# Performance work log

Measured on AMD Instinct MI355X. Metric: run time of the kernel, lower is better.

Reference implementation:

```python
import jax, jax.numpy as jnp
import numpy as np

N = 8192      # total QM atoms (concatenated over batch)
L = 6         # num_interactions / trajectory length
F = 256       # hidden_size
FH = F // 2
D_RBF = 32    # distance_embedding_size
E = 131072    # total probe edges
P = 32768     # total probes
CUTOFF = 4.0


def silu(x):
    return x * jax.nn.sigmoid(x)


def setup_inputs() -> dict:
    key = jax.random.key(0)
    ks = jax.random.split(key, 20)
    g = lambda k, shp, s=1.0: jax.random.normal(k, shp, dtype=jnp.float32) * s
    s_stack = g(ks[0], (N, L, F))
    v_stack = g(ks[1], (N, L, 3, F))
    # positions in a 2A box so all probe-atom distances < cutoff=4A
    atom_xyz = jax.random.uniform(ks[2], (N, 3), dtype=jnp.float32) * 2.0
    probe_xyz = jax.random.uniform(ks[3], (P, 3), dtype=jnp.float32) * 2.0
    cell = jnp.eye(3, dtype=jnp.float32) * 2.0
    probe_edges_displacement = jnp.zeros((E, 3), dtype=jnp.float32)
    atom_idx = jax.random.randint(ks[4], (E,), 0, N)
    probe_idx = jax.random.randint(ks[5], (E,), 0, P)
    probe_edges = jnp.stack([atom_idx, probe_idx], axis=1)
    in_dim = D_RBF + 3 * F  # e_pi || q_pi || n_i || S_JK
    return {
        's_stack': s_stack,
        'v_stack': v_stack,
        'atom_xyz': atom_xyz,
        'probe_xyz': probe_xyz,
        'cell': cell,
        'probe_edges_displacement': probe_edges_displacement,
        # JK attention MLP: F -> F/2 -> 1
        'attn_w1': g(ks[6], (F, FH), 1.0 / np.sqrt(F)),
        'attn_b1': jnp.zeros((FH,), jnp.float32),
        'attn_w2': g(ks[7], (FH, 1), 1.0 / np.sqrt(FH)),
        'attn_b2': jnp.zeros((1,), jnp.float32),
        # readout msg MLP: (D_rbf+3F) -> F -> F/2 -> 1
        'msg_w1': g(ks[8], (in_dim, F), 1.0 / np.sqrt(in_dim)),
        'msg_b1': jnp.zeros((F,), jnp.float32),
        'msg_w2': g(ks[9], (F, FH), 1.0 / np.sqrt(F)),
        'msg_b2': jnp.zeros((FH,), jnp.float32),
        'msg_w3': g(ks[10], (FH, 1), 1.0 / np.sqrt(FH)),
        'msg_b3': jnp.zeros((1,), jnp.float32),
        'probe_edges': probe_edges,
    }


def reference(s_stack, v_stack, atom_xyz, probe_xyz, cell, probe_edges_displacement,
              attn_w1, attn_b1, attn_w2, attn_b2,
              msg_w1, msg_b1, msg_w2, msg_b2, msg_w3, msg_b3,
              probe_edges):
    # ---- JKNetAggregation: node-level attention over layer trajectory ----
    h = silu(jnp.einsum('nlf,fh->nlh', s_stack, attn_w1) + attn_b1)   # [N,L,F/2]
    logits = (jnp.einsum('nlh,ho->nlo', h, attn_w2) + attn_b2)[..., 0]  # [N,L]
    a = jax.nn.softmax(logits, axis=1)                                  # [N,L]
    S_JK = jnp.einsum('nl,nlf->nf', a, s_stack)                         # [N,F]
    V_JK = jnp.einsum('nl,nlcf->ncf', a, v_stack)                       # [N,3,F]

    # ---- InfoBottleneckReadout: gather -> per-edge MLP -> scatter ----
    atom_idx = probe_edges[:, 0]
    probe_idx = probe_edges[:, 1]
    shift = probe_edges_displacement @ cell                             # [E,3] PBC shift
    diff = probe_xyz[probe_idx] - (atom_xyz[atom_idx] + shift)          # [E,3]
    dist = jnp.linalg.norm(diff, axis=-1)                               # [E]
    d = dist[:, None]
    n = jnp.arange(1, D_RBF + 1, dtype=jnp.float32)
    e_pi = jnp.sin(d * n * jnp.pi / CUTOFF) / (d + 1e-8)                # [E,D_rbf] sinc RBF
    r_hat = diff / (d + 1e-8)                                           # [E,3]
    V_e = V_JK[atom_idx]                                                # [E,3,F]
    q_pi = jnp.einsum('ecf,ec->ef', V_e, r_hat)                         # [E,F]
    n_i = jnp.linalg.norm(V_JK, axis=1)                                 # [N,F]
    h_pi = jnp.concatenate([e_pi, q_pi, n_i[atom_idx], S_JK[atom_idx]], axis=-1)  # [E,D_rbf+3F]
    m = silu(h_pi @ msg_w1 + msg_b1)
    m = silu(m @ msg_w2 + msg_b2)
    m = (m @ msg_w3 + msg_b3)[:, 0]                                     # [E]
    cw = jnp.where(dist < CUTOFF, 0.5 * (jnp.cos(jnp.pi * dist / CUTOFF) + 1.0), 0.0)
    rho = jax.ops.segment_sum(m * cw, probe_idx, num_segments=P)        # [P]
    return rho
```

## Files before the change

### kernel.cpp

```cpp
#include <hip/hip_runtime.h>
#include <math.h>
#include <stdint.h>


#define L_DIM 6
#define F_DIM 256
#define FH_DIM 128
#define DRBF 32
#define CUTOFF_F 4.0f
#define PI_F 3.14159265358979323846f

using bf16x8 = __attribute__((ext_vector_type(8))) short;
using f32x4v = __attribute__((ext_vector_type(4))) float;

__device__ __forceinline__ float silu_f(float x){ return x / (1.f + __expf(-x)); }

__device__ __forceinline__ unsigned short f2bf(float f){
    uint32_t u = __float_as_uint(f);
    uint32_t r = (u + 0x7fffu + ((u >> 16) & 1u)) >> 16;
    return (unsigned short)r;
}

__global__ __launch_bounds__(256) void kPrep(
    const float* __restrict__ msg_w1, const float* __restrict__ msg_w2,
    const float* __restrict__ attn_w1,
    unsigned short* __restrict__ w1bt, unsigned short* __restrict__ w1cdt,
    unsigned short* __restrict__ w2t, unsigned short* __restrict__ wA1t)
{
    int idx = blockIdx.x * 256 + threadIdx.x;
    if (idx < 65536){
        int k = idx >> 8, j = idx & 255;
        w1bt[(size_t)j * 256 + k] = f2bf(msg_w1[(size_t)(DRBF + k) * F_DIM + j]);
    } else if (idx < 196608){
        int i2 = idx - 65536;
        int k = i2 >> 8, j = i2 & 255;
        w1cdt[(size_t)j * 512 + k] = f2bf(msg_w1[(size_t)(DRBF + 256 + k) * F_DIM + j]);
    } else if (idx < 229376){
        int i3 = idx - 196608;
        int k = i3 >> 7, h = i3 & 127;
        w2t[(size_t)h * 256 + k] = f2bf(msg_w2[(size_t)k * FH_DIM + h]);
    } else {
        int i4 = idx - 229376;
        int j = i4 >> 8, k = i4 & 255;
        wA1t[(size_t)j * 256 + k] = f2bf(attn_w1[(size_t)k * FH_DIM + j]);
    }
}

__global__ __launch_bounds__(256) void kL(
    const float* __restrict__ s2d, const unsigned short* __restrict__ wA1t,
    const float* __restrict__ attn_b1, const float* __restrict__ attn_w2,
    float* __restrict__ LG)
{
    __shared__ float part[4][64];

    const int t  = threadIdx.x;
    const int l  = t & 63;
    const int w  = t >> 6;
    const int lm = l & 15, lq = l >> 4;

    bf16x8 bfr[2][8];
    #pragma unroll
    for (int nt2 = 0; nt2 < 2; nt2++){
        const int col = w*32 + nt2*16 + lm;
        #pragma unroll
        for (int kb = 0; kb < 8; kb++)
            bfr[nt2][kb] = *(const bf16x8*)(wA1t + (size_t)col * 256 + kb*32 + lq*8);
    }
    const float b1a = attn_b1[w*32 + lm];
    const float b1b = attn_b1[w*32 + 16 + lm];
    const float w2a = attn_w2[w*32 + lm];
    const float w2b = attn_w2[w*32 + 16 + lm];

    const int r00 = blockIdx.x * 64;

    #pragma unroll
    for (int mt = 0; mt < 4; mt++){
        const int r0 = r00 + mt * 16;
        bf16x8 af[8];
        #pragma unroll
        for (int kb = 0; kb < 8; kb++){
            const float* ap = s2d + (size_t)(r0 + lm) * 256 + kb*32 + lq*8;
            float4 fa = *(const float4*)ap;
            float4 fb = *(const float4*)(ap + 4);
            bf16x8 v;
            v[0] = (short)f2bf(fa.x); v[1] = (short)f2bf(fa.y);
            v[2] = (short)f2bf(fa.z); v[3] = (short)f2bf(fa.w);
            v[4] = (short)f2bf(fb.x); v[5] = (short)f2bf(fb.y);
            v[6] = (short)f2bf(fb.z); v[7] = (short)f2bf(fb.w);
            af[kb] = v;
        }
        f32x4v a0 = {0.f,0.f,0.f,0.f}, a1 = {0.f,0.f,0.f,0.f};
        #pragma unroll
        for (int kb = 0; kb < 8; kb++){
            a0 = __builtin_amdgcn_mfma_f32_16x16x32_bf16(af[kb], bfr[0][kb], a0, 0, 0, 0);
            a1 = __builtin_amdgcn_mfma_f32_16x16x32_bf16(af[kb], bfr[1][kb], a1, 0, 0, 0);
        }
        #pragma unroll
        for (int r = 0; r < 4; r++){
            float p = silu_f(a0[r] + b1a) * w2a + silu_f(a1[r] + b1b) * w2b;
            #pragma unroll
            for (int m = 8; m >= 1; m >>= 1) p += __shfl_xor(p, m, 64);
            if (lm == 0) part[w][mt*16 + lq*4 + r] = p;
        }
    }
    __syncthreads();
    if (t < 64)
        LG[r00 + t] = part[0][t] + part[1][t] + part[2][t] + part[3][t];
}

__global__ __launch_bounds__(256) void kW(
    const float* __restrict__ s_stack, const float* __restrict__ v_stack,
    const float* __restrict__ LG,
    unsigned short* __restrict__ VJKb, unsigned short* __restrict__ NISb, int N)
{
    const int t    = threadIdx.x;
    const int w    = t >> 6;
    const int lane = t & 63;
    const int n    = min(blockIdx.x * 4 + w, N - 1);

    float aw[L_DIM];
    #pragma unroll
    for (int l = 0; l < L_DIM; l++) aw[l] = LG[(size_t)n * L_DIM + l];
    float mx = aw[0];
    #pragma unroll
    for (int l = 1; l < L_DIM; l++) mx = fmaxf(mx, aw[l]);
    float sum = 0.f;
    #pragma unroll
    for (int l = 0; l < L_DIM; l++){ aw[l] = __expf(aw[l] - mx); sum += aw[l]; }
    const float inv = 1.f / sum;
    #pragma unroll
    for (int l = 0; l < L_DIM; l++) aw[l] *= inv;

    const float* sp = s_stack + (size_t)n * (L_DIM * F_DIM) + lane * 4;
    const float* vp = v_stack + (size_t)n * (L_DIM * 3 * F_DIM) + lane * 4;
    float4 v0 = {0.f,0.f,0.f,0.f}, v1 = {0.f,0.f,0.f,0.f}, v2 = {0.f,0.f,0.f,0.f};
    float4 sj = {0.f,0.f,0.f,0.f};
    #pragma unroll
    for (int l = 0; l < L_DIM; l++){
        const float a = aw[l];
        float4 ss = *(const float4*)(sp + (size_t)l * F_DIM);
        float4 x0 = *(const float4*)(vp + (size_t)(l*3+0) * F_DIM);
        float4 x1 = *(const float4*)(vp + (size_t)(l*3+1) * F_DIM);
        float4 x2 = *(const float4*)(vp + (size_t)(l*3+2) * F_DIM);
        v0.x = fmaf(a, x0.x, v0.x); v0.y = fmaf(a, x0.y, v0.y);
        v0.z = fmaf(a, x0.z, v0.z); v0.w = fmaf(a, x0.w, v0.w);
        v1.x = fmaf(a, x1.x, v1.x); v1.y = fmaf(a, x1.y, v1.y);
        v1.z = fmaf(a, x1.z, v1.z); v1.w = fmaf(a, x1.w, v1.w);
        v2.x = fmaf(a, x2.x, v2.x); v2.y = fmaf(a, x2.y, v2.y);
        v2.z = fmaf(a, x2.z, v2.z); v2.w = fmaf(a, x2.w, v2.w);
        sj.x = fmaf(a, ss.x, sj.x); sj.y = fmaf(a, ss.y, sj.y);
        sj.z = fmaf(a, ss.z, sj.z); sj.w = fmaf(a, ss.w, sj.w);
    }
    float4 ni;
    ni.x = sqrtf(v0.x*v0.x + v1.x*v1.x + v2.x*v2.x);
    ni.y = sqrtf(v0.y*v0.y + v1.y*v1.y + v2.y*v2.y);
    ni.z = sqrtf(v0.z*v0.z + v1.z*v1.z + v2.z*v2.z);
    ni.w = sqrtf(v0.w*v0.w + v1.w*v1.w + v2.w*v2.w);

    ushort4 o;
    o = (ushort4){f2bf(v0.x), f2bf(v0.y), f2bf(v0.z), f2bf(v0.w)};
    *(ushort4*)&VJKb[((size_t)n*3 + 0) * F_DIM + lane*4] = o;
    o = (ushort4){f2bf(v1.x), f2bf(v1.y), f2bf(v1.z), f2bf(v1.w)};
    *(ushort4*)&VJKb[((size_t)n*3 + 1) * F_DIM + lane*4] = o;
    o = (ushort4){f2bf(v2.x), f2bf(v2.y), f2bf(v2.z), f2bf(v2.w)};
    *(ushort4*)&VJKb[((size_t)n*3 + 2) * F_DIM + lane*4] = o;
    o = (ushort4){f2bf(ni.x), f2bf(ni.y), f2bf(ni.z), f2bf(ni.w)};
    *(ushort4*)&NISb[(size_t)n * 512 + lane*4] = o;
    o = (ushort4){f2bf(sj.x), f2bf(sj.y), f2bf(sj.z), f2bf(sj.w)};
    *(ushort4*)&NISb[(size_t)n * 512 + 256 + lane*4] = o;
}

__global__ __launch_bounds__(256) void kA2u(
    const unsigned short* __restrict__ VJKb, const unsigned short* __restrict__ w1bt,
    float* __restrict__ UT4, int M)
{
    const int t  = threadIdx.x;
    const int l  = t & 63;
    const int w  = t >> 6;
    const int lm = l & 15, lq = l >> 4;

    bf16x8 bfr[4][8];
    #pragma unroll
    for (int ct = 0; ct < 4; ct++)
        #pragma unroll
        for (int kb = 0; kb < 8; kb++)
            bfr[ct][kb] = *(const bf16x8*)(w1bt + (size_t)(w*64 + ct*16 + lm) * 256 + kb*32 + lq*8);

    const int r00 = blockIdx.x * 128;
    #pragma unroll 1
    for (int mt = 0; mt < 8; mt++){
        const int r0 = r00 + mt * 16;
        bf16x8 af[8];
        #pragma unroll
        for (int kb = 0; kb < 8; kb++)
            af[kb] = *(const bf16x8*)(VJKb + (size_t)(r0 + lm) * 256 + kb*32 + lq*8);
        f32x4v acc[4];
        #pragma unroll
        for (int ct = 0; ct < 4; ct++) acc[ct] = (f32x4v){0.f,0.f,0.f,0.f};
        #pragma unroll
        for (int kb = 0; kb < 8; kb++)
            #pragma unroll
            for (int ct = 0; ct < 4; ct++)
                acc[ct] = __builtin_amdgcn_mfma_f32_16x16x32_bf16(af[kb], bfr[ct][kb], acc[ct], 0, 0, 0);
        #pragma unroll
        for (int ct = 0; ct < 4; ct++){
            const int col = w*64 + ct*16 + lm;
            #pragma unroll
            for (int r = 0; r < 4; r++){
                const int row = r0 + lq*4 + r;
                const int n = row / 3, c = row - n*3;
                UT4[(((size_t)n << 8) + col) * 4 + c] = acc[ct][r];
            }
        }
    }
}

__global__ __launch_bounds__(256) void kA2t(
    const unsigned short* __restrict__ NISb, const unsigned short* __restrict__ w1cdt,
    const float* __restrict__ msg_b1,
    float* __restrict__ UT4, int M)
{
    const int t  = threadIdx.x;
    const int l  = t & 63;
    const int w  = t >> 6;
    const int lm = l & 15, lq = l >> 4;

    const int ch = blockIdx.x & 1;
    const int bm = blockIdx.x >> 1;

    bf16x8 bfr[2][16];
    #pragma unroll
    for (int ct = 0; ct < 2; ct++)
        #pragma unroll
        for (int kb = 0; kb < 16; kb++)
            bfr[ct][kb] = *(const bf16x8*)(w1cdt + (size_t)(ch*128 + w*32 + ct*16 + lm) * 512 + kb*32 + lq*8);

    const int r00 = bm * 128;
    #pragma unroll 1
    for (int mt = 0; mt < 8; mt++){
        const int r0 = r00 + mt * 16;
        bf16x8 af[16];
        #pragma unroll
        for (int kb = 0; kb < 16; kb++)
            af[kb] = *(const bf16x8*)(NISb + (size_t)(r0 + lm) * 512 + kb*32 + lq*8);
        f32x4v acc[2];
        #pragma unroll
        for (int ct = 0; ct < 2; ct++) acc[ct] = (f32x4v){0.f,0.f,0.f,0.f};
        #pragma unroll
        for (int kb = 0; kb < 16; kb++)
            #pragma unroll
            for (int ct = 0; ct < 2; ct++)
                acc[ct] = __builtin_amdgcn_mfma_f32_16x16x32_bf16(af[kb], bfr[ct][kb], acc[ct], 0, 0, 0);
        #pragma unroll
        for (int ct = 0; ct < 2; ct++){
            const int col = ch*128 + w*32 + ct*16 + lm;
            const float bias = msg_b1[col];
            #pragma unroll
            for (int r = 0; r < 4; r++){
                const int n = r0 + lq*4 + r;
                UT4[(((size_t)n << 8) + col) * 4 + 3] = acc[ct][r] + bias;
            }
        }
    }
}

__global__ __launch_bounds__(256) void kHist(const int* __restrict__ pe, int* __restrict__ cnt, int E){
    int e = blockIdx.x * 256 + threadIdx.x;
    if (e < E) atomicAdd(&cnt[pe[(size_t)e*2]], 1);
}

__global__ __launch_bounds__(1024) void kScan(const int* __restrict__ cnt, int* __restrict__ off, int N){
    __shared__ int sums[1024];
    const int t = threadIdx.x;
    const int base = t * 8;
    int c[8]; int s = 0;
    #pragma unroll
    for (int j = 0; j < 8; j++){
        int v = (base + j < N) ? cnt[base + j] : 0;
        c[j] = s; s += v;
    }
    sums[t] = s;
    __syncthreads();
    for (int d = 1; d < 1024; d <<= 1){
        int v = (t >= d) ? sums[t - d] : 0;
        __syncthreads();
        sums[t] += v;
        __syncthreads();
    }
    int excl = (t == 0) ? 0 : sums[t - 1];
    #pragma unroll
    for (int j = 0; j < 8; j++)
        if (base + j < N) off[base + j] = excl + c[j];
    if (t == 1023) off[N] = sums[1023];
}

__global__ __launch_bounds__(256) void kScatter(const int* __restrict__ pe,
    const int* __restrict__ off, int* __restrict__ pos, int* __restrict__ perm, int E){
    int e = blockIdx.x * 256 + threadIdx.x;
    if (e < E){
        int i = pe[(size_t)e*2];
        int slot = atomicAdd(&pos[i], 1);
        perm[off[i] + slot] = e;
    }
}

__global__ __launch_bounds__(256) void kB1(
    const int* __restrict__ pe, const float* __restrict__ disp,
    const float* __restrict__ cell,
    const float* __restrict__ atom_xyz, const float* __restrict__ probe_xyz,
    const float* __restrict__ UT4,
    const float* __restrict__ msg_w1,
    const unsigned short* __restrict__ w2t, const float* __restrict__ msg_b2,
    const float* __restrict__ msg_w3, const float* __restrict__ msg_b3,
    const int* __restrict__ perm,
    float* __restrict__ rho, int E)
{
    __shared__ unsigned short x_lds[32 * 256];
    __shared__ unsigned short epi_b[32 * 40];
    __shared__ int   ai_l[32];
    __shared__ int   pp_l[32];
    __shared__ float4 rc4_l[32];
    __shared__ float part[4][32];

    char* xbase = (char*)x_lds;

    const int t  = threadIdx.x;
    const int l  = t & 63;
    const int w  = t >> 6;
    const int lq = l >> 4;
    const int lm = l & 15;

    const float c0 = cell[0], c1 = cell[1], c2 = cell[2];
    const float c3 = cell[3], c4 = cell[4], c5 = cell[5];
    const float c6 = cell[6], c7 = cell[7], c8 = cell[8];

    bf16x8 w1afr[4];
    #pragma unroll
    for (int nt = 0; nt < 4; nt++){
        const int col = w*64 + nt*16 + lm;
        bf16x8 v;
        #pragma unroll
        for (int j = 0; j < 8; j++)
            v[j] = (short)f2bf(msg_w1[(size_t)(lq*8 + j) * F_DIM + col]);
        w1afr[nt] = v;
    }

    bf16x8 bfr[2][8];
    #pragma unroll
    for (int nt2 = 0; nt2 < 2; nt2++){
        const int h = w*32 + nt2*16 + lm;
        #pragma unroll
        for (int kb = 0; kb < 8; kb++)
            bfr[nt2][kb] = *(const bf16x8*)(w2t + (size_t)h * F_DIM + kb*32 + lq*8);
    }
    const float b2v0 = msg_b2[w*32 + lm];
    const float b2v1 = msg_b2[w*32 + 16 + lm];
    const float w3v0 = msg_w3[w*32 + lm];
    const float w3v1 = msg_w3[w*32 + 16 + lm];
    const float b3   = msg_b3[0];

    const int e0 = blockIdx.x * 128;

    int ee_r[4], ia_r[4], ip_r[4];
    #pragma unroll
    for (int bb = 0; bb < 4; bb++){
        int s = min(e0 + bb*32 + (t >> 3), E - 1);
        ee_r[bb] = perm[s];
    }
    #pragma unroll
    for (int bb = 0; bb < 4; bb++){
        ia_r[bb] = pe[(size_t)ee_r[bb]*2];
        ip_r[bb] = pe[(size_t)ee_r[bb]*2 + 1];
    }

    #pragma unroll 1
    for (int bb = 0; bb < 4; bb++){
        const int e0b = e0 + bb * 32;

        {
            const int slot = t >> 3, q = t & 7;
            const int ee = ee_r[bb];
            const int ia = ia_r[bb];
            const int ip = ip_r[bb];
            const float d0 = disp[(size_t)ee*3], d1 = disp[(size_t)ee*3+1], d2 = disp[(size_t)ee*3+2];
            const float sx = d0*c0 + d1*c3 + d2*c6;
            const float sy = d0*c1 + d1*c4 + d2*c7;
            const float sz = d0*c2 + d1*c5 + d2*c8;
            const float dx = probe_xyz[(size_t)ip*3+0] - (atom_xyz[(size_t)ia*3+0] + sx);
            const float dy = probe_xyz[(size_t)ip*3+1] - (atom_xyz[(size_t)ia*3+1] + sy);
            const float dz = probe_xyz[(size_t)ip*3+2] - (atom_xyz[(size_t)ia*3+2] + sz);
            const float dist = sqrtf(dx*dx + dy*dy + dz*dz);
            const float inv  = 1.f / (dist + 1e-8f);
            const float base = dist * (PI_F / CUTOFF_F);
            ushort4 eb;
            eb.x = f2bf(__sinf(base * (float)(q*4 + 1)) * inv);
            eb.y = f2bf(__sinf(base * (float)(q*4 + 2)) * inv);
            eb.z = f2bf(__sinf(base * (float)(q*4 + 3)) * inv);
            eb.w = f2bf(__sinf(base * (float)(q*4 + 4)) * inv);
            *(ushort4*)&epi_b[slot*40 + q*4] = eb;
            if (q == 0){
                ai_l[slot] = ia;
                pp_l[slot] = ip;
                float cw = (dist < CUTOFF_F) ? 0.5f * (__cosf(base) + 1.f) : 0.f;
                rc4_l[slot] = (float4){dx*inv, dy*inv, dz*inv, cw};
            }
        }
        __syncthreads();

        f32x4v pacc[2][4];
        #pragma unroll
        for (int mt = 0; mt < 2; mt++)
            #pragma unroll
            for (int nt = 0; nt < 4; nt++) pacc[mt][nt] = (f32x4v){0.f,0.f,0.f,0.f};
        #pragma unroll
        for (int mt = 0; mt < 2; mt++){
            const bf16x8 af = *(const bf16x8*)&epi_b[(mt*16 + lm)*40 + lq*8];
            #pragma unroll
            for (int nt = 0; nt < 4; nt++)
                pacc[mt][nt] = __builtin_amdgcn_mfma_f32_16x16x32_bf16(af, w1afr[nt], pacc[mt][nt], 0, 0, 0);
        }

        #pragma unroll
        for (int mt = 0; mt < 2; mt++){
            #pragma unroll
            for (int r = 0; r < 4; r++){
                const int e = mt*16 + lq*4 + r;
                const int i = ai_l[e];
                const float4 rc = rc4_l[e];
                const float* up = UT4 + ((size_t)i << 10);
                #pragma unroll
                for (int nt = 0; nt < 4; nt++){
                    const int col = w*64 + nt*16 + lm;
                    const float4 ut = *(const float4*)(up + (size_t)col * 4);
                    float z = pacc[mt][nt][r] + ut.w;
                    z = fmaf(rc.x, ut.x, fmaf(rc.y, ut.y, fmaf(rc.z, ut.z, z)));
                    const int wofs = e*512 + ((col*2) ^ ((e & 7) << 4));
                    *(unsigned short*)(xbase + wofs) = f2bf(silu_f(z));
                }
            }
        }
        __syncthreads();

        f32x4v acc00 = {0.f,0.f,0.f,0.f}, acc01 = {0.f,0.f,0.f,0.f};
        f32x4v acc10 = {0.f,0.f,0.f,0.f}, acc11 = {0.f,0.f,0.f,0.f};
        const int eA0 = lm;
        const int eA1 = 16 + lm;
        #pragma unroll
        for (int kb = 0; kb < 8; kb++){
            const int ko = kb*64 + lq*16;
            bf16x8 af0 = *(const bf16x8*)(xbase + eA0*512 + (ko ^ ((eA0 & 7) << 4)));
            bf16x8 af1 = *(const bf16x8*)(xbase + eA1*512 + (ko ^ ((eA1 & 7) << 4)));
            acc00 = __builtin_amdgcn_mfma_f32_16x16x32_bf16(af0, bfr[0][kb], acc00, 0, 0, 0);
            acc01 = __builtin_amdgcn_mfma_f32_16x16x32_bf16(af0, bfr[1][kb], acc01, 0, 0, 0);
            acc10 = __builtin_amdgcn_mfma_f32_16x16x32_bf16(af1, bfr[0][kb], acc10, 0, 0, 0);
            acc11 = __builtin_amdgcn_mfma_f32_16x16x32_bf16(af1, bfr[1][kb], acc11, 0, 0, 0);
        }

        float pr0[4], pr1[4];
        #pragma unroll
        for (int r = 0; r < 4; r++){
            pr0[r] = silu_f(acc00[r] + b2v0) * w3v0 + silu_f(acc01[r] + b2v1) * w3v1;
            pr1[r] = silu_f(acc10[r] + b2v0) * w3v0 + silu_f(acc11[r] + b2v1) * w3v1;
        }
        #pragma unroll
        for (int r = 0; r < 4; r++){
            #pragma unroll
            for (int m = 8; m >= 1; m >>= 1){
                pr0[r] += __shfl_xor(pr0[r], m, 64);
                pr1[r] += __shfl_xor(pr1[r], m, 64);
            }
        }
        if (lm == 0){
            #pragma unroll
            for (int r = 0; r < 4; r++){
                part[w][lq*4 + r]      = pr0[r];
                part[w][16 + lq*4 + r] = pr1[r];
            }
        }
        __syncthreads();

        if (t < 32 && (e0b + t) < E){
            float tot = part[0][t] + part[1][t] + part[2][t] + part[3][t] + b3;
            atomicAdd(&rho[pp_l[t]], tot * rc4_l[t].w);
        }
        __syncthreads();
    }
}

extern "C" void kernel_launch(void* const* d_in, const int* in_sizes, int n_in,
                              void* d_out, int out_size, void* d_ws, size_t ws_size,
                              hipStream_t stream)
{
    const float* s_stack   = (const float*)d_in[0];
    const float* v_stack   = (const float*)d_in[1];
    const float* atom_xyz  = (const float*)d_in[2];
    const float* probe_xyz = (const float*)d_in[3];
    const float* cell      = (const float*)d_in[4];
    const float* disp      = (const float*)d_in[5];
    const float* attn_w1   = (const float*)d_in[6];
    const float* attn_b1   = (const float*)d_in[7];
    const float* attn_w2   = (const float*)d_in[8];
    const float* msg_w1    = (const float*)d_in[10];
    const float* msg_b1    = (const float*)d_in[11];
    const float* msg_w2    = (const float*)d_in[12];
    const float* msg_b2    = (const float*)d_in[13];
    const float* msg_w3    = (const float*)d_in[14];
    const float* msg_b3    = (const float*)d_in[15];
    const int*   pe        = (const int*)d_in[16];

    const int N = in_sizes[0] / (L_DIM * F_DIM);
    const int E = in_sizes[16] / 2;
    const int P = out_size;
    const size_t NF = (size_t)N * F_DIM;

    float* ws = (float*)d_ws;
    unsigned short* VJKb = (unsigned short*)ws;
    unsigned short* NISb = VJKb + 3*NF;
    float* UT4 = ws + (5*NF)/2;
    unsigned short* w1bt  = (unsigned short*)(ws + (13*NF)/2);
    unsigned short* w1cdt = w1bt + 65536;
    unsigned short* w2t   = w1cdt + 131072;
    unsigned short* wA1t  = w2t + 32768;
    float* LG  = (float*)(wA1t + 32768);
    int* cnt  = (int*)(LG + (size_t)N * L_DIM);
    int* pos  = cnt + N;
    int* offs = pos + N;
    int* perm = offs + N + 1;

    hipMemsetAsync(d_out, 0, (size_t)P * sizeof(float), stream);
    hipMemsetAsync(cnt, 0, 2 * (size_t)N * sizeof(int), stream);

    kPrep<<<1024, 256, 0, stream>>>(msg_w1, msg_w2, attn_w1, w1bt, w1cdt, w2t, wA1t);

    kL<<<(N * L_DIM) / 64, 256, 0, stream>>>(s_stack, wA1t, attn_b1, attn_w2, LG);
    kW<<<(N + 3) / 4, 256, 0, stream>>>(s_stack, v_stack, LG, VJKb, NISb, N);

    kA2u<<<(3 * N) / 128, 256, 0, stream>>>(VJKb, w1bt, UT4, 3 * N);
    kA2t<<<(N / 128) * 2, 256, 0, stream>>>(NISb, w1cdt, msg_b1, UT4, N);

    const int gE = (E + 255) / 256;
    kHist<<<gE, 256, 0, stream>>>(pe, cnt, E);
    kScan<<<1, 1024, 0, stream>>>(cnt, offs, N);
    kScatter<<<gE, 256, 0, stream>>>(pe, offs, pos, perm, E);

    kB1<<<(E + 127) / 128, 256, 0, stream>>>(pe, disp, cell, atom_xyz, probe_xyz,
                                             UT4, msg_w1,
                                             w2t, msg_b2, msg_w3, msg_b3,
                                             perm, (float*)d_out, E);
}
```

Baseline: 208.1 us.

## Fuse attention logits with JK weighting, merge A2 GEMMs, fold memsets into prep

Merges the layer-attention logit kernel and the weighted JK aggregation kernel into one kernel. The logits for 16 atoms stay in shared memory, which removes the LG buffer round trip and one launch. The two first-layer projection GEMM kernels now run as one launch that branches on block index. The output and count memsets move into the weight prep kernel. This cuts launch overhead and global traffic, but the fused kernel has fewer blocks, so there is less parallelism in the aggregation phase.

Result: faster. 190.4 us (-8.5%).

```diff
diff --git a/kernel.cpp b/kernel.cpp
--- a/kernel.cpp
+++ b/kernel.cpp
@@ -25,7 +25,8 @@
     const float* __restrict__ msg_w1, const float* __restrict__ msg_w2,
     const float* __restrict__ attn_w1,
     unsigned short* __restrict__ w1bt, unsigned short* __restrict__ w1cdt,
-    unsigned short* __restrict__ w2t, unsigned short* __restrict__ wA1t)
+    unsigned short* __restrict__ w2t, unsigned short* __restrict__ wA1t,
+    float* __restrict__ rho, int P, int* __restrict__ cntpos, int CN)
 {
     int idx = blockIdx.x * 256 + threadIdx.x;
     if (idx < 65536){
@@ -39,19 +40,27 @@
         int i3 = idx - 196608;
         int k = i3 >> 7, h = i3 & 127;
         w2t[(size_t)h * 256 + k] = f2bf(msg_w2[(size_t)k * FH_DIM + h]);
-    } else {
+    } else if (idx < 262144){
         int i4 = idx - 229376;
         int j = i4 >> 8, k = i4 & 255;
         wA1t[(size_t)j * 256 + k] = f2bf(attn_w1[(size_t)k * FH_DIM + j]);
-    }
-}
-
-__global__ __launch_bounds__(256) void kL(
-    const float* __restrict__ s2d, const unsigned short* __restrict__ wA1t,
+    } else if (idx < 262144 + 32768){
+        int i5 = idx - 262144;
+        if (i5 < P) rho[i5] = 0.f;
+    } else {
+        int i6 = idx - 262144 - 32768;
+        if (i6 < CN) cntpos[i6] = 0;
+    }
+}
+
+__global__ __launch_bounds__(256) void kAW(
+    const float* __restrict__ s_stack, const float* __restrict__ v_stack,
+    const unsigned short* __restrict__ wA1t,
     const float* __restrict__ attn_b1, const float* __restrict__ attn_w2,
-    float* __restrict__ LG)
+    unsigned short* __restrict__ VJKb, unsigned short* __restrict__ NISb, int N)
 {
-    __shared__ float part[4][64];
+    __shared__ float part[4][96];
+    __shared__ float aw_l[16][8];
 
     const int t  = threadIdx.x;
     const int l  = t & 63;
@@ -71,15 +80,18 @@
     const float w2a = attn_w2[w*32 + lm];
     const float w2b = attn_w2[w*32 + 16 + lm];
 
-    const int r00 = blockIdx.x * 64;
-
-    #pragma unroll
-    for (int mt = 0; mt < 4; mt++){
-        const int r0 = r00 + mt * 16;
+    const int n0 = blockIdx.x * 16;
+    const size_t rbase = (size_t)n0 * L_DIM;
+    const size_t rmax  = (size_t)N * L_DIM - 1;
+
+    #pragma unroll
+    for (int mt = 0; mt < 6; mt++){
+        const size_t r0 = rbase + mt * 16;
         bf16x8 af[8];
         #pragma unroll
         for (int kb = 0; kb < 8; kb++){
-            const float* ap = s2d + (size_t)(r0 + lm) * 256 + kb*32 + lq*8;
+            size_t row = r0 + lm; if (row > rmax) row = rmax;
+            const float* ap = s_stack + row * 256 + kb*32 + lq*8;
             float4 fa = *(const float4*)ap;
             float4 fb = *(const float4*)(ap + 4);
             bf16x8 v;
@@ -104,161 +116,151 @@
         }
     }
     __syncthreads();
-    if (t < 64)
-        LG[r00 + t] = part[0][t] + part[1][t] + part[2][t] + part[3][t];
-}
-
-__global__ __launch_bounds__(256) void kW(
-    const float* __restrict__ s_stack, const float* __restrict__ v_stack,
-    const float* __restrict__ LG,
-    unsigned short* __restrict__ VJKb, unsigned short* __restrict__ NISb, int N)
-{
-    const int t    = threadIdx.x;
-    const int w    = t >> 6;
-    const int lane = t & 63;
-    const int n    = min(blockIdx.x * 4 + w, N - 1);
-
-    float aw[L_DIM];
-    #pragma unroll
-    for (int l = 0; l < L_DIM; l++) aw[l] = LG[(size_t)n * L_DIM + l];
-    float mx = aw[0];
-    #pragma unroll
-    for (int l = 1; l < L_DIM; l++) mx = fmaxf(mx, aw[l]);
-    float sum = 0.f;
-    #pragma unroll
-    for (int l = 0; l < L_DIM; l++){ aw[l] = __expf(aw[l] - mx); sum += aw[l]; }
-    const float inv = 1.f / sum;
-    #pragma unroll
-    for (int l = 0; l < L_DIM; l++) aw[l] *= inv;
-
-    const float* sp = s_stack + (size_t)n * (L_DIM * F_DIM) + lane * 4;
-    const float* vp = v_stack + (size_t)n * (L_DIM * 3 * F_DIM) + lane * 4;
-    float4 v0 = {0.f,0.f,0.f,0.f}, v1 = {0.f,0.f,0.f,0.f}, v2 = {0.f,0.f,0.f,0.f};
-    float4 sj = {0.f,0.f,0.f,0.f};
-    #pragma unroll
-    for (int l = 0; l < L_DIM; l++){
-        const float a = aw[l];
-        float4 ss = *(const float4*)(sp + (size_t)l * F_DIM);
-        float4 x0 = *(const float4*)(vp + (size_t)(l*3+0) * F_DIM);
-        float4 x1 = *(const float4*)(vp + (size_t)(l*3+1) * F_DIM);
-        float4 x2 = *(const float4*)(vp + (size_t)(l*3+2) * F_DIM);
-        v0.x = fmaf(a, x0.x, v0.x); v0.y = fmaf(a, x0.y, v0.y);
-        v0.z = fmaf(a, x0.z, v0.z); v0.w = fmaf(a, x0.w, v0.w);
-        v1.x = fmaf(a, x1.x, v1.x); v1.y = fmaf(a, x1.y, v1.y);
-        v1.z = fmaf(a, x1.z, v1.z); v1.w = fmaf(a, x1.w, v1.w);
-        v2.x = fmaf(a, x2.x, v2.x); v2.y = fmaf(a, x2.y, v2.y);
-        v2.z = fmaf(a, x2.z, v2.z); v2.w = fmaf(a, x2.w, v2.w);
-        sj.x = fmaf(a, ss.x, sj.x); sj.y = fmaf(a, ss.y, sj.y);
-        sj.z = fmaf(a, ss.z, sj.z); sj.w = fmaf(a, ss.w, sj.w);
-    }
-    float4 ni;
-    ni.x = sqrtf(v0.x*v0.x + v1.x*v1.x + v2.x*v2.x);
-    ni.y = sqrtf(v0.y*v0.y + v1.y*v1.y + v2.y*v2.y);
-    ni.z = sqrtf(v0.z*v0.z + v1.z*v1.z + v2.z*v2.z);
-    ni.w = sqrtf(v0.w*v0.w + v1.w*v1.w + v2.w*v2.w);
-
-    ushort4 o;
-    o = (ushort4){f2bf(v0.x), f2bf(v0.y), f2bf(v0.z), f2bf(v0.w)};
-    *(ushort4*)&VJKb[((size_t)n*3 + 0) * F_DIM + lane*4] = o;
-    o = (ushort4){f2bf(v1.x), f2bf(v1.y), f2bf(v1.z), f2bf(v1.w)};
-    *(ushort4*)&VJKb[((size_t)n*3 + 1) * F_DIM + lane*4] = o;
-    o = (ushort4){f2bf(v2.x), f2bf(v2.y), f2bf(v2.z), f2bf(v2.w)};
-    *(ushort4*)&VJKb[((size_t)n*3 + 2) * F_DIM + lane*4] = o;
-    o = (ushort4){f2bf(ni.x), f2bf(ni.y), f2bf(ni.z), f2bf(ni.w)};
-    *(ushort4*)&NISb[(size_t)n * 512 + lane*4] = o;
-    o = (ushort4){f2bf(sj.x), f2bf(sj.y), f2bf(sj.z), f2bf(sj.w)};
-    *(ushort4*)&NISb[(size_t)n * 512 + 256 + lane*4] = o;
-}
-
-__global__ __launch_bounds__(256) void kA2u(
+    if (t < 96) part[0][t] = part[0][t] + part[1][t] + part[2][t] + part[3][t];
+    __syncthreads();
+    if (t < 16){
+        float e[L_DIM]; float mx = -1e30f;
+        #pragma unroll
+        for (int l6 = 0; l6 < L_DIM; l6++) mx = fmaxf(mx, part[0][t*L_DIM + l6]);
+        float s = 0.f;
+        #pragma unroll
+        for (int l6 = 0; l6 < L_DIM; l6++){ e[l6] = __expf(part[0][t*L_DIM + l6] - mx); s += e[l6]; }
+        float inv = 1.f / s;
+        #pragma unroll
+        for (int l6 = 0; l6 < L_DIM; l6++) aw_l[t][l6] = e[l6] * inv;
+    }
+    __syncthreads();
+
+    #pragma unroll 1
+    for (int aa = 0; aa < 4; aa++){
+        const int n = min(n0 + w*4 + aa, N - 1);
+        float aw[L_DIM];
+        #pragma unroll
+        for (int l6 = 0; l6 < L_DIM; l6++) aw[l6] = aw_l[w*4 + aa][l6];
+
+        const float* sp = s_stack + (size_t)n * (L_DIM * F_DIM) + l * 4;
+        const float* vp = v_stack + (size_t)n * (L_DIM * 3 * F_DIM) + l * 4;
+        float4 v0 = {0.f,0.f,0.f,0.f}, v1 = {0.f,0.f,0.f,0.f}, v2 = {0.f,0.f,0.f,0.f};
+        float4 sj = {0.f,0.f,0.f,0.f};
+        #pragma unroll
+        for (int l6 = 0; l6 < L_DIM; l6++){
+            const float a = aw[l6];
+            float4 ss = *(const float4*)(sp + (size_t)l6 * F_DIM);
+            float4 x0 = *(const float4*)(vp + (size_t)(l6*3+0) * F_DIM);
+            float4 x1 = *(const float4*)(vp + (size_t)(l6*3+1) * F_DIM);
+            float4 x2 = *(const float4*)(vp + (size_t)(l6*3+2) * F_DIM);
+            v0.x = fmaf(a, x0.x, v0.x); v0.y = fmaf(a, x0.y, v0.y);
+            v0.z = fmaf(a, x0.z, v0.z); v0.w = fmaf(a, x0.w, v0.w);
+            v1.x = fmaf(a, x1.x, v1.x); v1.y = fmaf(a, x1.y, v1.y);
+            v1.z = fmaf(a, x1.z, v1.z); v1.w = fmaf(a, x1.w, v1.w);
+            v2.x = fmaf(a, x2.x, v2.x); v2.y = fmaf(a, x2.y, v2.y);
+            v2.z = fmaf(a, x2.z, v2.z); v2.w = fmaf(a, x2.w, v2.w);
+            sj.x = fmaf(a, ss.x, sj.x); sj.y = fmaf(a, ss.y, sj.y);
+            sj.z = fmaf(a, ss.z, sj.z); sj.w = fmaf(a, ss.w, sj.w);
+        }
+        float4 ni;
+        ni.x = sqrtf(v0.x*v0.x + v1.x*v1.x + v2.x*v2.x);
+        ni.y = sqrtf(v0.y*v0.y + v1.y*v1.y + v2.y*v2.y);
+        ni.z = sqrtf(v0.z*v0.z + v1.z*v1.z + v2.z*v2.z);
+        ni.w = sqrtf(v0.w*v0.w + v1.w*v1.w + v2.w*v2.w);
+
+        ushort4 o;
+        o = (ushort4){f2bf(v0.x), f2bf(v0.y), f2bf(v0.z), f2bf(v0.w)};
+        *(ushort4*)&VJKb[((size_t)n*3 + 0) * F_DIM + l*4] = o;
+        o = (ushort4){f2bf(v1.x), f2bf(v1.y), f2bf(v1.z), f2bf(v1.w)};
+        *(ushort4*)&VJKb[((size_t)n*3 + 1) * F_DIM + l*4] = o;
+        o = (ushort4){f2bf(v2.x), f2bf(v2.y), f2bf(v2.z), f2bf(v2.w)};
+        *(ushort4*)&VJKb[((size_t)n*3 + 2) * F_DIM + l*4] = o;
+        o = (ushort4){f2bf(ni.x), f2bf(ni.y), f2bf(ni.z), f2bf(ni.w)};
+        *(ushort4*)&NISb[(size_t)n * 512 + l*4] = o;
+        o = (ushort4){f2bf(sj.x), f2bf(sj.y), f2bf(sj.z), f2bf(sj.w)};
+        *(ushort4*)&NISb[(size_t)n * 512 + 256 + l*4] = o;
+    }
+}
+
+__global__ __launch_bounds__(256) void kA2(
     const unsigned short* __restrict__ VJKb, const unsigned short* __restrict__ w1bt,
-    float* __restrict__ UT4, int M)
+    const unsigned short* __restrict__ NISb, const unsigned short* __restrict__ w1cdt,
+    const float* __restrict__ msg_b1,
+    float* __restrict__ UT4, int gU)
 {
     const int t  = threadIdx.x;
     const int l  = t & 63;
     const int w  = t >> 6;
     const int lm = l & 15, lq = l >> 4;
 
-    bf16x8 bfr[4][8];
-    #pragma unroll
-    for (int ct = 0; ct < 4; ct++)
-        #pragma unroll
-        for (int kb = 0; kb < 8; kb++)
-            bfr[ct][kb] = *(const bf16x8*)(w1bt + (size_t)(w*64 + ct*16 + lm) * 256 + kb*32 + lq*8);
-
-    const int r00 = blockIdx.x * 128;
-    #pragma unroll 1
-    for (int mt = 0; mt < 8; mt++){
-        const int r0 = r00 + mt * 16;
-        bf16x8 af[8];
-        #pragma unroll
-        for (int kb = 0; kb < 8; kb++)
-            af[kb] = *(const bf16x8*)(VJKb + (size_t)(r0 + lm) * 256 + kb*32 + lq*8);
-        f32x4v acc[4];
-        #pragma unroll
-        for (int ct = 0; ct < 4; ct++) acc[ct] = (f32x4v){0.f,0.f,0.f,0.f};
-        #pragma unroll
-        for (int kb = 0; kb < 8; kb++)
-            #pragma unroll
-            for (int ct = 0; ct < 4; ct++)
-                acc[ct] = __builtin_amdgcn_mfma_f32_16x16x32_bf16(af[kb], bfr[ct][kb], acc[ct], 0, 0, 0);
-        #pragma unroll
-        for (int ct = 0; ct < 4; ct++){
-            const int col = w*64 + ct*16 + lm;
-            #pragma unroll
-            for (int r = 0; r < 4; r++){
-                const int row = r0 + lq*4 + r;
-                const int n = row / 3, c = row - n*3;
-                UT4[(((size_t)n << 8) + col) * 4 + c] = acc[ct][r];
+    if ((int)blockIdx.x < gU){
+        bf16x8 bfr[4][8];
+        #pragma unroll
+        for (int ct = 0; ct < 4; ct++)
+            #pragma unroll
+            for (int kb = 0; kb < 8; kb++)
+                bfr[ct][kb] = *(const bf16x8*)(w1bt + (size_t)(w*64 + ct*16 + lm) * 256 + kb*32 + lq*8);
+
+        const int r00 = blockIdx.x * 128;
+        #pragma unroll 1
+        for (int mt = 0; mt < 8; mt++){
+            const int r0 = r00 + mt * 16;
+            bf16x8 af[8];
+            #pragma unroll
+            for (int kb = 0; kb < 8; kb++)
+                af[kb] = *(const bf16x8*)(VJKb + (size_t)(r0 + lm) * 256 + kb*32 + lq*8);
+            f32x4v acc[4];
+            #pragma unroll
+            for (int ct = 0; ct < 4; ct++) acc[ct] = (f32x4v){0.f,0.f,0.f,0.f};
+            #pragma unroll
+            for (int kb = 0; kb < 8; kb++)
+                #pragma unroll
+                for (int ct = 0; ct < 4; ct++)
+                    acc[ct] = __builtin_amdgcn_mfma_f32_16x16x32_bf16(af[kb], bfr[ct][kb], acc[ct], 0, 0, 0);
+            #pragma unroll
+            for (int ct = 0; ct < 4; ct++){
+                const int col = w*64 + ct*16 + lm;
+                #pragma unroll
+                for (int r = 0; r < 4; r++){
+                    const int row = r0 + lq*4 + r;
+                    const int n = row / 3, c = row - n*3;
+                    UT4[(((size_t)n << 8) + col) * 4 + c] = acc[ct][r];
+                }
             }
         }
-    }
-}
-
-__global__ __launch_bounds__(256) void kA2t(
-    const unsigned short* __restrict__ NISb, const unsigned short* __restrict__ w1cdt,
-    const float* __restrict__ msg_b1,
-    float* __restrict__ UT4, int M)
-{
-    const int t  = threadIdx.x;
-    const int l  = t & 63;
-    const int w  = t >> 6;
-    const int lm = l & 15, lq = l >> 4;
-
-    const int ch = blockIdx.x & 1;
-    const int bm = blockIdx.x >> 1;
-
-    bf16x8 bfr[2][16];
-    #pragma unroll
-    for (int ct = 0; ct < 2; ct++)
-        #pragma unroll
-        for (int kb = 0; kb < 16; kb++)
-            bfr[ct][kb] = *(const bf16x8*)(w1cdt + (size_t)(ch*128 + w*32 + ct*16 + lm) * 512 + kb*32 + lq*8);
-
-    const int r00 = bm * 128;
-    #pragma unroll 1
-    for (int mt = 0; mt < 8; mt++){
-        const int r0 = r00 + mt * 16;
-        bf16x8 af[16];
-        #pragma unroll
-        for (int kb = 0; kb < 16; kb++)
-            af[kb] = *(const bf16x8*)(NISb + (size_t)(r0 + lm) * 512 + kb*32 + lq*8);
-        f32x4v acc[2];
-        #pragma unroll
-        for (int ct = 0; ct < 2; ct++) acc[ct] = (f32x4v){0.f,0.f,0.f,0.f};
-        #pragma unroll
-        for (int kb = 0; kb < 16; kb++)
-            #pragma unroll
-            for (int ct = 0; ct < 2; ct++)
-                acc[ct] = __builtin_amdgcn_mfma_f32_16x16x32_bf16(af[kb], bfr[ct][kb], acc[ct], 0, 0, 0);
-        #pragma unroll
-        for (int ct = 0; ct < 2; ct++){
-            const int col = ch*128 + w*32 + ct*16 + lm;
-            const float bias = msg_b1[col];
-            #pragma unroll
-            for (int r = 0; r < 4; r++){
-                const int n = r0 + lq*4 + r;
-                UT4[(((size_t)n << 8) + col) * 4 + 3] = acc[ct][r] + bias;
+    } else {
+        const int bid = blockIdx.x - gU;
+        const int ch = bid & 1;
+        const int bm = bid >> 1;
+
+        bf16x8 bfr[2][16];
+        #pragma unroll
+        for (int ct = 0; ct < 2; ct++)
+            #pragma unroll
+            for (int kb = 0; kb < 16; kb++)
+                bfr[ct][kb] = *(const bf16x8*)(w1cdt + (size_t)(ch*128 + w*32 + ct*16 + lm) * 512 + kb*32 + lq*8);
+
+        const int r00 = bm * 128;
+        #pragma unroll 1
+        for (int mt = 0; mt < 8; mt++){
+            const int r0 = r00 + mt * 16;
+            bf16x8 af[16];
+            #pragma unroll
+            for (int kb = 0; kb < 16; kb++)
+                af[kb] = *(const bf16x8*)(NISb + (size_t)(r0 + lm) * 512 + kb*32 + lq*8);
+            f32x4v acc[2];
+            #pragma unroll
+            for (int ct = 0; ct < 2; ct++) acc[ct] = (f32x4v){0.f,0.f,0.f,0.f};
+            #pragma unroll
+            for (int kb = 0; kb < 16; kb++)
+                #pragma unroll
+                for (int ct = 0; ct < 2; ct++)
+                    acc[ct] = __builtin_amdgcn_mfma_f32_16x16x32_bf16(af[kb], bfr[ct][kb], acc[ct], 0, 0, 0);
+            #pragma unroll
+            for (int ct = 0; ct < 2; ct++){
+                const int col = ch*128 + w*32 + ct*16 + lm;
+                const float bias = msg_b1[col];
+                #pragma unroll
+                for (int r = 0; r < 4; r++){
+                    const int n = r0 + lq*4 + r;
+                    UT4[(((size_t)n << 8) + col) * 4 + 3] = acc[ct][r] + bias;
+                }
             }
         }
     }
@@ -521,22 +523,22 @@
     unsigned short* w1cdt = w1bt + 65536;
     unsigned short* w2t   = w1cdt + 131072;
     unsigned short* wA1t  = w2t + 32768;
-    float* LG  = (float*)(wA1t + 32768);
-    int* cnt  = (int*)(LG + (size_t)N * L_DIM);
+    int* cnt  = (int*)(wA1t + 32768);
     int* pos  = cnt + N;
     int* offs = pos + N;
     int* perm = offs + N + 1;
 
-    hipMemsetAsync(d_out, 0, (size_t)P * sizeof(float), stream);
-    hipMemsetAsync(cnt, 0, 2 * (size_t)N * sizeof(int), stream);
-
-    kPrep<<<1024, 256, 0, stream>>>(msg_w1, msg_w2, attn_w1, w1bt, w1cdt, w2t, wA1t);
-
-    kL<<<(N * L_DIM) / 64, 256, 0, stream>>>(s_stack, wA1t, attn_b1, attn_w2, LG);
-    kW<<<(N + 3) / 4, 256, 0, stream>>>(s_stack, v_stack, LG, VJKb, NISb, N);
-
-    kA2u<<<(3 * N) / 128, 256, 0, stream>>>(VJKb, w1bt, UT4, 3 * N);
-    kA2t<<<(N / 128) * 2, 256, 0, stream>>>(NISb, w1cdt, msg_b1, UT4, N);
+    const int prepElems = 262144 + 32768 + 2 * N;
+    kPrep<<<(prepElems + 255) / 256, 256, 0, stream>>>(
+        msg_w1, msg_w2, attn_w1, w1bt, w1cdt, w2t, wA1t,
+        (float*)d_out, P, cnt, 2 * N);
+
+    kAW<<<(N + 15) / 16, 256, 0, stream>>>(s_stack, v_stack, wA1t, attn_b1, attn_w2,
+                                           VJKb, NISb, N);
+
+    const int gU = (3 * N) / 128;
+    const int gT = (N / 128) * 2;
+    kA2<<<gU + gT, 256, 0, stream>>>(VJKb, w1bt, NISb, w1cdt, msg_b1, UT4, gU);
 
     const int gE = (E + 255) / 256;
     kHist<<<gE, 256, 0, stream>>>(pe, cnt, E);
```
